# Kernel tuning notes

Hardware: AMD Instinct MI355X
Metric: run time of the kernel (lower is better)

## Reference

```python
import jax, jax.numpy as jnp
import numpy as np
from jax import lax


def squash(vec):
    # vec: [..., caps, dim]; squash along last dim (dim=2 in original layout [B, caps, dim])
    lensq = jnp.sum(vec * vec, axis=2)
    length = jnp.sqrt(lensq)
    scale = (lensq / (1.0 + lensq) / length)[:, :, None]
    return vec * scale


def setup_inputs() -> dict:
    key = jax.random.key(0)
    ks = jax.random.split(key, 6)
    stdv = 1.0 / np.sqrt(1152.0)
    return {
        "x": jax.random.normal(ks[0], (512, 1, 28, 28), dtype=jnp.float32),
        "conv1_w": jax.random.normal(ks[1], (256, 1, 9, 9), dtype=jnp.float32) * 0.05,
        "conv1_b": jax.random.normal(ks[2], (256,), dtype=jnp.float32) * 0.01,
        "conv2_w": jax.random.normal(ks[3], (256, 256, 9, 9), dtype=jnp.float32) * 0.01,
        "conv2_b": jax.random.normal(ks[4], (256,), dtype=jnp.float32) * 0.01,
        "caps_w": jax.random.uniform(ks[5], (1152, 8, 160), dtype=jnp.float32, minval=-stdv, maxval=stdv),
        "b_prior": jnp.zeros((1152, 10), dtype=jnp.float32),
    }


def reference(x, conv1_w, conv1_b, conv2_w, conv2_b, caps_w, b_prior):
    n_iterations = 3
    output_caps, output_dim = 10, 16
    dn = ("NCHW", "OIHW", "NCHW")

    # conv1 + relu: [N,1,28,28] -> [N,256,20,20]
    h = lax.conv_general_dilated(x, conv1_w, (1, 1), "VALID", dimension_numbers=dn)
    h = jax.nn.relu(h + conv1_b[None, :, None, None])

    # first capsule layer: conv k=9 s=2 -> [N,256,6,6]
    h = lax.conv_general_dilated(h, conv2_w, (2, 2), "VALID", dimension_numbers=dn)
    h = h + conv2_b[None, :, None, None]
    N, C, H, W = h.shape
    # [N, 32, 8, H, W] -> [N, 32, H, W, 8] -> [N, 32*H*W, 8]
    u = h.reshape(N, 32, 8, H, W).transpose(0, 1, 3, 4, 2).reshape(N, 32 * H * W, 8)
    u = squash(u)  # [N, 1152, 8]

    # prediction vectors: u_hat [N, 1152, 10, 16]
    u_hat = jnp.einsum("bid,ido->bio", u, caps_w).reshape(N, 1152, output_caps, output_dim)

    # dynamic routing-by-agreement
    c = jax.nn.softmax(b_prior, axis=1)  # [1152, 10]
    s = jnp.sum(c[None, :, :, None] * u_hat, axis=1)  # [N, 10, 16]
    v = squash(s)
    b_batch = jnp.broadcast_to(b_prior, (N, 1152, output_caps))
    for _ in range(n_iterations):
        b_batch = b_batch + jnp.sum(u_hat * v[:, None, :, :], axis=-1)  # agreement
        c = jax.nn.softmax(b_batch, axis=2)[..., None]  # [N, 1152, 10, 1]
        s = jnp.sum(c * u_hat, axis=1)
        v = squash(s)

    probs = jnp.sqrt(jnp.sum(v * v, axis=2))  # [N, 10]
    return (v, probs)
```

## Files before the change

kernel.cpp:

```cpp
#include <hip/hip_runtime.h>


#define N_IMG 512

typedef __attribute__((ext_vector_type(8))) short bf16x8;
typedef __attribute__((ext_vector_type(4))) float f32x4;
typedef __attribute__((ext_vector_type(4))) unsigned int u32x4;

__device__ __forceinline__ unsigned short f2bf(float v) {
  unsigned int uu = __float_as_uint(v);
  uu += 0x7FFF + ((uu >> 16) & 1);
  return (unsigned short)(uu >> 16);
}
__device__ __forceinline__ float bf2f(unsigned short h) {
  return __uint_as_float(((unsigned int)h) << 16);
}
__device__ __forceinline__ int swz16(int row) {
  return (row ^ ((row >> 3) & 7)) << 4;
}

__global__ __launch_bounds__(256) void repack_b_kernel(
    const float* __restrict__ w2, unsigned short* __restrict__ bph,
    unsigned short* __restrict__ bpl) {
  __shared__ float slab[82 * 16 * 17];
  const int n = blockIdx.x, c = blockIdx.y;
  const int tid = threadIdx.x;
  for (int e = tid; e < 81 * 256; e += 256) {
    const int row = e / 81;
    const int rs = e - row * 81;
    const int co = row >> 4, ci = row & 15;
    slab[(rs * 16 + co) * 17 + ci] =
        w2[((size_t)(n * 16 + co) * 256 + c * 16 + ci) * 81 + rs];
  }
  __syncthreads();
  const int lane = tid & 63;
  const int l15 = lane & 15;
  const int lh = lane >> 5;
  const int cio8 = ((lane >> 4) & 1) * 8;
  for (int tt = tid >> 6; tt < 41; tt += 4) {
    const int rs = 2 * tt + lh;
    unsigned int hw[4], lw[4];
#pragma unroll
    for (int jp = 0; jp < 4; ++jp) {
      unsigned short h2[2], l2[2];
#pragma unroll
      for (int e = 0; e < 2; ++e) {
        const int j = jp * 2 + e;
        float v = (rs < 81) ? slab[(rs * 16 + l15) * 17 + cio8 + j] : 0.0f;
        unsigned short hh = f2bf(v);
        h2[e] = hh;
        l2[e] = f2bf(v - bf2f(hh));
      }
      hw[jp] = (unsigned int)h2[0] | ((unsigned int)h2[1] << 16);
      lw[jp] = (unsigned int)l2[0] | ((unsigned int)l2[1] << 16);
    }
    const size_t off = (((size_t)n * 656 + c * 41 + tt) * 64 + lane) * 8;
    *(u32x4*)(bph + off) = (u32x4){hw[0], hw[1], hw[2], hw[3]};
    *(u32x4*)(bpl + off) = (u32x4){lw[0], lw[1], lw[2], lw[3]};
  }
}

__global__ __launch_bounds__(160) void repack_cw_kernel(
    const float* __restrict__ cw, float* __restrict__ cwt) {
  __shared__ float t[8][160];
  const int i = blockIdx.x;
  const int od = threadIdx.x;
#pragma unroll
  for (int k = 0; k < 8; ++k) t[k][od] = cw[((size_t)i * 8 + k) * 160 + od];
  __syncthreads();
  float4 o0 = {t[0][od], t[1][od], t[2][od], t[3][od]};
  float4 o1 = {t[4][od], t[5][od], t[6][od], t[7][od]};
  float4* dst = (float4*)(cwt + ((size_t)i * 160 + od) * 8);
  dst[0] = o0;
  dst[1] = o1;
}

__global__ __launch_bounds__(256) void c0_kernel(const float* __restrict__ bp,
                                                 float* __restrict__ c0b) {
  const int i = blockIdx.x * 256 + threadIdx.x;
  if (i >= 1152) return;
  float b[10];
  float m = -1e30f;
#pragma unroll
  for (int o = 0; o < 10; ++o) {
    b[o] = bp[i * 10 + o];
    m = fmaxf(m, b[o]);
  }
  float sum = 0.0f;
#pragma unroll
  for (int o = 0; o < 10; ++o) {
    b[o] = __expf(b[o] - m);
    sum += b[o];
  }
  const float inv = 1.0f / sum;
#pragma unroll
  for (int o = 0; o < 10; ++o) c0b[i * 10 + o] = b[o] * inv;
}

__global__ __launch_bounds__(256) void gemm_s0_kernel(
    const float* __restrict__ u, const float* __restrict__ cw,
    const float* __restrict__ c0b, float* __restrict__ s0p) {
  __shared__ float a_l[64 * 257];
  __shared__ float b_l[64 * 160];
  __shared__ float c0_l[320];
  const int mt = blockIdx.x;
  const int ks = blockIdx.y;
  const int m0 = mt * 64;
  const int tid = threadIdx.x;
  const int mb = tid >> 4;
  const int ob = (tid & 15) * 10;

  for (int i = tid; i < 320; i += 256) c0_l[i] = c0b[(ks * 32) * 10 + i];
  for (int idx = tid; idx < 16384; idx += 256) {
    const int m = idx >> 8, kk = idx & 255;
    a_l[m * 257 + kk] = u[(size_t)(m0 + m) * 9216 + ks * 256 + kk];
  }

  float acc[4][10];
#pragma unroll
  for (int r = 0; r < 4; ++r)
#pragma unroll
    for (int c = 0; c < 10; ++c) acc[r][c] = 0.0f;

#pragma unroll 1
  for (int kc = 0; kc < 4; ++kc) {
    __syncthreads();
    for (int idx = tid; idx < 10240; idx += 256) {
      const int kk = idx / 160, od = idx - kk * 160;
      const int kg = kc * 64 + kk;
      b_l[kk * 160 + od] = cw[((size_t)ks * 256 + kg) * 160 + od] *
                           c0_l[(kg >> 3) * 10 + (od >> 4)];
    }
    __syncthreads();
#pragma unroll 4
    for (int kk = 0; kk < 64; ++kk) {
      float a4[4];
#pragma unroll
      for (int r = 0; r < 4; ++r)
        a4[r] = a_l[(mb * 4 + r) * 257 + kc * 64 + kk];
      const float* bp_ = &b_l[kk * 160 + ob];
#pragma unroll
      for (int c = 0; c < 10; ++c) {
        const float bv = bp_[c];
#pragma unroll
        for (int r = 0; r < 4; ++r) acc[r][c] = fmaf(a4[r], bv, acc[r][c]);
      }
    }
  }

#pragma unroll
  for (int r = 0; r < 4; ++r) {
#pragma unroll
    for (int c = 0; c < 10; ++c) {
      s0p[((size_t)ks * N_IMG + m0 + mb * 4 + r) * 160 + ob + c] = acc[r][c];
    }
  }
}

template <int H>
__device__ __forceinline__ void conv1_half(const float* __restrict__ ib,
                                           const float* __restrict__ w1l,
                                           float* __restrict__ stg, int ch,
                                           int oy, float bv1) {
  float a[10];
#pragma unroll
  for (int ox = 0; ox < 10; ++ox) a[ox] = bv1;
#pragma unroll
  for (int r = 0; r < 9; ++r) {
    float row[20];
    const float4* rp = (const float4*)&ib[(oy + r) * 28 + H * 8];
#pragma unroll
    for (int q = 0; q < 5; ++q) {
      float4 v4 = rp[q];
      row[4 * q + 0] = v4.x; row[4 * q + 1] = v4.y;
      row[4 * q + 2] = v4.z; row[4 * q + 3] = v4.w;
    }
#pragma unroll
    for (int s = 0; s < 9; ++s) {
      const float wval = w1l[ch * 81 + r * 9 + s];
#pragma unroll
      for (int ox = 0; ox < 10; ++ox)
        a[ox] = fmaf(row[ox + s + 2 * H], wval, a[ox]);
    }
  }
  float2* dst = (float2*)&stg[oy * 20 + H * 10];
#pragma unroll
  for (int q = 0; q < 5; ++q) {
    float2 v2;
    v2.x = fmaxf(a[2 * q + 0], 0.0f);
    v2.y = fmaxf(a[2 * q + 1], 0.0f);
    dst[q] = v2;
  }
}

__global__ __launch_bounds__(512, 1) void fused_conv_kernel(
    const float* __restrict__ x, const float* __restrict__ w1,
    const float* __restrict__ b1, const unsigned short* __restrict__ bph,
    const unsigned short* __restrict__ bpl, const float* __restrict__ b2,
    float* __restrict__ u) {
  __shared__ __align__(16) char smem[115008];
  float* stg = (float*)(smem + 51776);
  float* img = (float*)(smem + 103488);
  float* w1l = (float*)(smem + 109760);
  float* b1l = (float*)(smem + 114944);
  float* mrg = (float*)smem;
  float* sq = (float*)smem;

  const int bp2 = blockIdx.x;
  const int tid = threadIdx.x;
  const int wid = tid >> 6;
  const int g = wid & 3;
  const int kpar = wid >> 2;
  const int lane = tid & 63;
  const int l15 = lane & 15;
  const int lq4 = lane >> 4;
  const int lqb = lq4 & 1;
  const int lh = lane >> 5;

  int rowb[5];
  bool okm[5];
#pragma unroll
  for (int mt = 0; mt < 5; ++mt) {
    const int m = mt * 16 + l15;
    okm[mt] = (m < 72);
    const int mm = okm[mt] ? m : 0;
    const int im = (mm >= 36) ? 1 : 0;
    const int p = mm - 36 * im;
    const int oy = p / 6, ox = p - 6 * oy;
    rowb[mt] = im * 400 + 40 * oy + 2 * ox;
  }

  for (int i = tid; i < 1568; i += 512) img[i] = x[bp2 * 1568 + i];
  if (tid < 16) {
    *(int*)(smem + (tid >> 2) * 12944 + 804 * 16 + (tid & 3) * 4) = 0;
  }

  f32x4 acc[5][4];
#pragma unroll
  for (int mt = 0; mt < 5; ++mt)
#pragma unroll
    for (int nn = 0; nn < 4; ++nn) acc[mt][nn] = (f32x4){0.f, 0.f, 0.f, 0.f};

  const char* hbase = smem + lqb * 12944;
  const char* lbase = smem + 25888 + lqb * 12944;
  const int tt0 = kpar ? 21 : 0;
  const int tt1 = kpar ? 41 : 21;
  const int nk = tt1 - tt0;

#define MFMA_STEP(CBH, CBL, J, DOPF)                                       \
  {                                                                        \
    const int rs_ = 2 * (tt0 + (J)) + lh;                                  \
    const int r_ = (rs_ * 57) >> 9;                                        \
    const int s_ = rs_ - 9 * r_;                                           \
    const int rs20_ = 20 * r_ + s_;                                        \
    const bool okrs_ = (rs_ <= 80);                                        \
    bf16x8 ah[5], al[5];                                                   \
    _Pragma("unroll") for (int mt = 0; mt < 5; ++mt) {                     \
      const int row_ = (okm[mt] && okrs_) ? (rowb[mt] + rs20_) : 800;      \
      const int ad_ = swz16(row_);                                         \
      ah[mt] = *(const bf16x8*)(hbase + ad_);                              \
      al[mt] = *(const bf16x8*)(lbase + ad_);                              \
    }                                                                      \
    _Pragma("unroll") for (int mt = 0; mt < 5; ++mt) {                     \
      _Pragma("unroll") for (int nn = 0; nn < 4; ++nn) {                   \
        acc[mt][nn] = __builtin_amdgcn_mfma_f32_16x16x32_bf16(             \
            al[mt], CBH[nn], acc[mt][nn], 0, 0, 0);                        \
        acc[mt][nn] = __builtin_amdgcn_mfma_f32_16x16x32_bf16(             \
            ah[mt], CBL[nn], acc[mt][nn], 0, 0, 0);                        \
        acc[mt][nn] = __builtin_amdgcn_mfma_f32_16x16x32_bf16(             \
            ah[mt], CBH[nn], acc[mt][nn], 0, 0, 0);                        \
      }                                                                    \
    }                                                                      \
    if ((DOPF) && (J) + 2 < nk) {                                          \
      _Pragma("unroll") for (int nn = 0; nn < 4; ++nn) {                   \
        CBH[nn] = *(const bf16x8*)(pb[nn] + (size_t)((J) + 2) * 512);      \
        CBL[nn] = *(const bf16x8*)(pl[nn] + (size_t)((J) + 2) * 512);      \
      }                                                                    \
    }                                                                      \
  }

#pragma unroll 1
  for (int c = 0; c < 16; ++c) {
    const unsigned short* pb[4];
    const unsigned short* pl[4];
#pragma unroll
    for (int nn = 0; nn < 4; ++nn) {
      const size_t base =
          ((size_t)(g * 4 + nn) * 656 + c * 41 + tt0) * 512 + lane * 8;
      pb[nn] = bph + base;
      pl[nn] = bpl + base;
    }
    bf16x8 cbh0[4], cbl0[4], cbh1[4], cbl1[4];
#pragma unroll
    for (int nn = 0; nn < 4; ++nn) {
      cbh0[nn] = *(const bf16x8*)(pb[nn]);
      cbl0[nn] = *(const bf16x8*)(pl[nn]);
      cbh1[nn] = *(const bf16x8*)(pb[nn] + 512);
      cbl1[nn] = *(const bf16x8*)(pl[nn] + 512);
    }

    __syncthreads();
    for (int i = tid; i < 1296; i += 512) w1l[i] = w1[c * 1296 + i];
    if (tid < 16) b1l[tid] = b1[c * 16 + tid];
    __syncthreads();

    for (int t = tid; t < 1280; t += 512) {
      const int half = (t >= 640) ? 1 : 0;
      const int rest = t - half * 640;
      const int ig = rest / 320;
      const int r2 = rest - ig * 320;
      const int ch = r2 & 15;
      const int oy = r2 >> 4;
      const float* ib = &img[ig * 784];
      float* sb = &stg[(ig * 16 + ch) * 404];
      const float bv1 = b1l[ch];
      if (half == 0)
        conv1_half<0>(ib, w1l, sb, ch, oy, bv1);
      else
        conv1_half<1>(ib, w1l, sb, ch, oy, bv1);
    }
    __syncthreads();

    for (int t = tid; t < 800; t += 512) {
      const int ig = t / 400;
      const int pos = t - ig * 400;
      const int ad = swz16(t);
      unsigned int hw[8], lw[8];
#pragma unroll
      for (int jp = 0; jp < 8; ++jp) {
        unsigned short h2[2], l2[2];
#pragma unroll
        for (int e = 0; e < 2; ++e) {
          const float v = stg[(ig * 16 + jp * 2 + e) * 404 + pos];
          const unsigned short hh = f2bf(v);
          h2[e] = hh;
          l2[e] = f2bf(v - bf2f(hh));
        }
        hw[jp] = (unsigned int)h2[0] | ((unsigned int)h2[1] << 16);
        lw[jp] = (unsigned int)l2[0] | ((unsigned int)l2[1] << 16);
      }
      *(u32x4*)(smem + ad) = (u32x4){hw[0], hw[1], hw[2], hw[3]};
      *(u32x4*)(smem + 12944 + ad) = (u32x4){hw[4], hw[5], hw[6], hw[7]};
      *(u32x4*)(smem + 25888 + ad) = (u32x4){lw[0], lw[1], lw[2], lw[3]};
      *(u32x4*)(smem + 38832 + ad) = (u32x4){lw[4], lw[5], lw[6], lw[7]};
    }
    __syncthreads();

    int j = 0;
#pragma unroll 1
    for (; j + 1 < nk; j += 2) {
      MFMA_STEP(cbh0, cbl0, j, 1);
      MFMA_STEP(cbh1, cbl1, j + 1, 1);
    }
    if (j < nk) MFMA_STEP(cbh0, cbl0, j, 0);
  }
#undef MFMA_STEP

  __syncthreads();
  if (kpar == 1) {
#pragma unroll
    for (int mt = 0; mt < 5; ++mt)
#pragma unroll
      for (int nn = 0; nn < 4; ++nn)
        *(f32x4*)(mrg + ((((g * 5 + mt) * 4 + nn) * 64 + lane) << 2)) =
            acc[mt][nn];
  }
  __syncthreads();
  if (kpar == 0) {
#pragma unroll
    for (int mt = 0; mt < 5; ++mt)
#pragma unroll
      for (int nn = 0; nn < 4; ++nn)
        acc[mt][nn] +=
            *(const f32x4*)(mrg + ((((g * 5 + mt) * 4 + nn) * 64 + lane) << 2));
  }
  __syncthreads();
  if (kpar == 0) {
    float b2v[4];
#pragma unroll
    for (int nn = 0; nn < 4; ++nn) b2v[nn] = b2[(g * 4 + nn) * 16 + l15];
#pragma unroll
    for (int mt = 0; mt < 5; ++mt) {
#pragma unroll
      for (int i = 0; i < 4; ++i) {
        const int m = mt * 16 + lq4 * 4 + i;
        if (m < 72) {
          const int im = (m >= 36) ? 1 : 0;
          const int p36 = m - 36 * im;
#pragma unroll
          for (int nn = 0; nn < 4; ++nn) {
            sq[(im * 256 + (g * 4 + nn) * 16 + l15) * 36 + p36] =
                acc[mt][nn][i] + b2v[nn];
          }
        }
      }
    }
  }
  __syncthreads();

  for (int i = tid; i < 2304; i += 512) {
    const int ig = i / 1152;
    const int cap = i - ig * 1152;
    const int gg = cap / 36, yx = cap - 36 * gg;
    float vals[8];
    float lensq = 0.0f;
#pragma unroll
    for (int d = 0; d < 8; ++d) {
      vals[d] = sq[(ig * 256 + gg * 8 + d) * 36 + yx];
      lensq = fmaf(vals[d], vals[d], lensq);
    }
    const float len = sqrtf(lensq);
    const float scale = lensq / (1.0f + lensq) / len;
    float4* dst = (float4*)(u + ((size_t)(bp2 * 2 + ig) * 1152 + cap) * 8);
    float4 lo4, hi4;
    lo4.x = vals[0] * scale; lo4.y = vals[1] * scale;
    lo4.z = vals[2] * scale; lo4.w = vals[3] * scale;
    hi4.x = vals[4] * scale; hi4.y = vals[5] * scale;
    hi4.z = vals[6] * scale; hi4.w = vals[7] * scale;
    dst[0] = lo4; dst[1] = hi4;
  }
}

__global__ __launch_bounds__(256) void routing_a_kernel(
    const float* __restrict__ u, const float* __restrict__ cwt,
    const float* __restrict__ b_prior, const float* __restrict__ vsum,
    float* __restrict__ s_part, int pass) {
  __shared__ float u_l[64 * 8];
  __shared__ float uhat[64 * 160];
  __shared__ float b_l[64 * 10];
  __shared__ float c_l[64 * 10];
  __shared__ float v_l[160];

  const int b = blockIdx.x;
  const int ch = blockIdx.y;
  const int cap0 = ch * 64;
  const int tid = threadIdx.x;

  {
    const float* src = u + ((size_t)b * 1152 + cap0) * 8;
    for (int i = tid; i < 512; i += 256) u_l[i] = src[i];
  }
  if (pass > 0 && tid < 160) v_l[tid] = vsum[b * 160 + tid];
  __syncthreads();

  for (int idx = tid; idx < 64 * 160; idx += 256) {
    const int i = idx / 160, od = idx - 160 * i;
    const float4* wp =
        (const float4*)(cwt + ((size_t)(cap0 + i) * 160 + od) * 8);
    const float4 wa = wp[0], wb = wp[1];
    const float4 ua = *(const float4*)&u_l[i * 8];
    const float4 ub = *(const float4*)&u_l[i * 8 + 4];
    float a = ua.x * wa.x;
    a = fmaf(ua.y, wa.y, a); a = fmaf(ua.z, wa.z, a); a = fmaf(ua.w, wa.w, a);
    a = fmaf(ub.x, wb.x, a); a = fmaf(ub.y, wb.y, a);
    a = fmaf(ub.z, wb.z, a); a = fmaf(ub.w, wb.w, a);
    uhat[idx] = a;
  }
  __syncthreads();

  for (int idx = tid; idx < 640; idx += 256) {
    const int i = idx / 10, o = idx - 10 * i;
    float bb = b_prior[(cap0 + i) * 10 + o];
    if (pass > 0) {
      float agg = 0.0f;
#pragma unroll
      for (int d = 0; d < 16; ++d)
        agg = fmaf(uhat[i * 160 + o * 16 + d], v_l[o * 16 + d], agg);
      bb += agg;
    }
    b_l[idx] = bb;
  }
  __syncthreads();

  if (tid < 64) {
    float m = -1e30f;
#pragma unroll
    for (int o = 0; o < 10; ++o) m = fmaxf(m, b_l[tid * 10 + o]);
    float e[10], sum = 0.0f;
#pragma unroll
    for (int o = 0; o < 10; ++o) {
      e[o] = __expf(b_l[tid * 10 + o] - m);
      sum += e[o];
    }
    const float inv = 1.0f / sum;
#pragma unroll
    for (int o = 0; o < 10; ++o) c_l[tid * 10 + o] = e[o] * inv;
  }
  __syncthreads();

  if (tid < 160) {
    const int o = tid / 16;
    float a = 0.0f;
    for (int i = 0; i < 64; ++i)
      a = fmaf(c_l[i * 10 + o], uhat[i * 160 + tid], a);
    s_part[((size_t)ch * N_IMG + b) * 160 + tid] = a;
  }
}

__global__ __launch_bounds__(192) void routing_b_kernel(
    const float* __restrict__ s_part, int nchunk, float* __restrict__ v_out,
    float* __restrict__ probs, float* __restrict__ vsum, int mode) {
  __shared__ float s_l[160];
  __shared__ float scale_l[10];
  __shared__ float len_l[10];
  const int b = blockIdx.x;
  const int t = threadIdx.x;
  if (t < 160) {
    float a = 0.0f;
    for (int ch = 0; ch < nchunk; ++ch)
      a += s_part[((size_t)ch * N_IMG + b) * 160 + t];
    s_l[t] = a;
  }
  __syncthreads();
  if (t < 10) {
    float lensq = 0.0f;
#pragma unroll
    for (int d = 0; d < 16; ++d) {
      const float xv = s_l[t * 16 + d];
      lensq = fmaf(xv, xv, lensq);
    }
    const float len = sqrtf(lensq);
    scale_l[t] = lensq / (1.0f + lensq) / len;
    len_l[t] = lensq / (1.0f + lensq);
  }
  __syncthreads();
  if (t < 160) {
    const float vv = s_l[t] * scale_l[t / 16];
    v_out[b * 160 + t] = vv;
    if (mode == 0) vsum[b * 160 + t] = vv;
    else if (mode == 1) vsum[b * 160 + t] += vv;
  }
  if (t < 10) probs[b * 10 + t] = len_l[t];
}

extern "C" void kernel_launch(void* const* d_in, const int* in_sizes, int n_in,
                              void* d_out, int out_size, void* d_ws,
                              size_t ws_size, hipStream_t stream) {
  const float* x  = (const float*)d_in[0];
  const float* w1 = (const float*)d_in[1];
  const float* b1 = (const float*)d_in[2];
  const float* w2 = (const float*)d_in[3];
  const float* b2 = (const float*)d_in[4];
  const float* cw = (const float*)d_in[5];
  const float* bp = (const float*)d_in[6];

  float* out = (float*)d_out;
  float* v_out = out;
  float* probs = out + N_IMG * 160;

  float* base = (float*)d_ws;
  unsigned short* bph = (unsigned short*)d_ws;
  unsigned short* bpl = bph + (size_t)16 * 656 * 512;
  float* u    = base + 5373952;
  float* sp   = u + 4718592;
  float* vsum = sp + 1474560;
  float* c0b  = vsum + 81920;
  float* cwt = base;
  float* s0p = base + 1474560;

  repack_b_kernel<<<dim3(16, 16), 256, 0, stream>>>(w2, bph, bpl);
  fused_conv_kernel<<<256, 512, 0, stream>>>(x, w1, b1, bph, bpl, b2, u);
  c0_kernel<<<5, 256, 0, stream>>>(bp, c0b);
  repack_cw_kernel<<<1152, 160, 0, stream>>>(cw, cwt);
  gemm_s0_kernel<<<dim3(8, 36), 256, 0, stream>>>(u, cw, c0b, s0p);
  routing_b_kernel<<<N_IMG, 192, 0, stream>>>(s0p, 36, v_out, probs, vsum, 0);
  for (int pass = 1; pass < 4; ++pass) {
    const int mode = (pass < 3) ? 1 : 2;
    routing_a_kernel<<<dim3(N_IMG, 18), 256, 0, stream>>>(u, cwt, bp, vsum, sp,
                                                          pass);
    routing_b_kernel<<<N_IMG, 192, 0, stream>>>(sp, 18, v_out, probs, vsum,
                                                mode);
  }
}
```

Baseline: 1.104 ms.

## Batch four images per routing block to reuse capsule weights across images

Each routing_a block now handles RG=4 images and 32 capsules, walked in two 16-capsule sub-chunks. Each loaded cwt weight vector is reused across the four images, so weight traffic per image drops. The padded uhat layout, with rows of 161, is meant to reduce LDS bank conflicts. The grid goes to 128x36 blocks with partial sums over 36 chunks, which adds more work to the reduction in routing_b and changes the workspace layout.

```diff
diff --git a/kernel.cpp b/kernel.cpp
--- a/kernel.cpp
+++ b/kernel.cpp
@@ -2,6 +2,7 @@
 
 
 #define N_IMG 512
+#define RG 4
 
 typedef __attribute__((ext_vector_type(8))) short bf16x8;
 typedef __attribute__((ext_vector_type(4))) float f32x4;
@@ -424,76 +425,106 @@
 __global__ __launch_bounds__(256) void routing_a_kernel(
     const float* __restrict__ u, const float* __restrict__ cwt,
     const float* __restrict__ b_prior, const float* __restrict__ vsum,
-    float* __restrict__ s_part, int pass) {
-  __shared__ float u_l[64 * 8];
-  __shared__ float uhat[64 * 160];
-  __shared__ float b_l[64 * 10];
-  __shared__ float c_l[64 * 10];
-  __shared__ float v_l[160];
-
-  const int b = blockIdx.x;
+    float* __restrict__ s_part) {
+  __shared__ float u_l[RG * 16 * 8];
+  __shared__ float uhat[RG][16][161];
+  __shared__ float v_l[RG * 160];
+  __shared__ float bp_l[32 * 10];
+  __shared__ float c_l[RG * 16 * 10];
+  __shared__ float s_acc[RG * 160];
+
+  const int gb = blockIdx.x;
   const int ch = blockIdx.y;
-  const int cap0 = ch * 64;
+  const int cap0 = ch * 32;
+  const int b0 = gb * RG;
   const int tid = threadIdx.x;
 
-  {
-    const float* src = u + ((size_t)b * 1152 + cap0) * 8;
-    for (int i = tid; i < 512; i += 256) u_l[i] = src[i];
-  }
-  if (pass > 0 && tid < 160) v_l[tid] = vsum[b * 160 + tid];
-  __syncthreads();
-
-  for (int idx = tid; idx < 64 * 160; idx += 256) {
-    const int i = idx / 160, od = idx - 160 * i;
-    const float4* wp =
-        (const float4*)(cwt + ((size_t)(cap0 + i) * 160 + od) * 8);
-    const float4 wa = wp[0], wb = wp[1];
-    const float4 ua = *(const float4*)&u_l[i * 8];
-    const float4 ub = *(const float4*)&u_l[i * 8 + 4];
-    float a = ua.x * wa.x;
-    a = fmaf(ua.y, wa.y, a); a = fmaf(ua.z, wa.z, a); a = fmaf(ua.w, wa.w, a);
-    a = fmaf(ub.x, wb.x, a); a = fmaf(ub.y, wb.y, a);
-    a = fmaf(ub.z, wb.z, a); a = fmaf(ub.w, wb.w, a);
-    uhat[idx] = a;
-  }
-  __syncthreads();
-
-  for (int idx = tid; idx < 640; idx += 256) {
-    const int i = idx / 10, o = idx - 10 * i;
-    float bb = b_prior[(cap0 + i) * 10 + o];
-    if (pass > 0) {
+  for (int i = tid; i < RG * 160; i += 256) {
+    const int g = i / 160, od = i - g * 160;
+    v_l[i] = vsum[(b0 + g) * 160 + od];
+    s_acc[i] = 0.0f;
+  }
+  for (int i = tid; i < 320; i += 256) bp_l[i] = b_prior[cap0 * 10 + i];
+
+#pragma unroll 1
+  for (int cc = 0; cc < 2; ++cc) {
+    const int c16 = cap0 + cc * 16;
+    __syncthreads();
+    for (int i = tid; i < RG * 128; i += 256) {
+      const int g = i >> 7, off = i & 127;
+      u_l[g * 128 + off] = u[((size_t)(b0 + g) * 1152 + c16) * 8 + off];
+    }
+    __syncthreads();
+
+    for (int e = tid; e < 2560; e += 256) {
+      const int i = e / 160, od = e - i * 160;
+      const float4* wp =
+          (const float4*)(cwt + ((size_t)(c16 + i) * 160 + od) * 8);
+      const float4 wa = wp[0], wb = wp[1];
+#pragma unroll
+      for (int g = 0; g < RG; ++g) {
+        const float* up = &u_l[(g * 16 + i) * 8];
+        float a = up[0] * wa.x;
+        a = fmaf(up[1], wa.y, a);
+        a = fmaf(up[2], wa.z, a);
+        a = fmaf(up[3], wa.w, a);
+        a = fmaf(up[4], wb.x, a);
+        a = fmaf(up[5], wb.y, a);
+        a = fmaf(up[6], wb.z, a);
+        a = fmaf(up[7], wb.w, a);
+        uhat[g][i][od] = a;
+      }
+    }
+    __syncthreads();
+
+    for (int e = tid; e < RG * 160; e += 256) {
+      const int g = e / 160;
+      const int r = e - g * 160;
+      const int i = r / 10, o = r - i * 10;
       float agg = 0.0f;
 #pragma unroll
       for (int d = 0; d < 16; ++d)
-        agg = fmaf(uhat[i * 160 + o * 16 + d], v_l[o * 16 + d], agg);
-      bb += agg;
-    }
-    b_l[idx] = bb;
-  }
-  __syncthreads();
-
-  if (tid < 64) {
-    float m = -1e30f;
-#pragma unroll
-    for (int o = 0; o < 10; ++o) m = fmaxf(m, b_l[tid * 10 + o]);
-    float e[10], sum = 0.0f;
-#pragma unroll
-    for (int o = 0; o < 10; ++o) {
-      e[o] = __expf(b_l[tid * 10 + o] - m);
-      sum += e[o];
-    }
-    const float inv = 1.0f / sum;
-#pragma unroll
-    for (int o = 0; o < 10; ++o) c_l[tid * 10 + o] = e[o] * inv;
-  }
-  __syncthreads();
-
-  if (tid < 160) {
-    const int o = tid / 16;
-    float a = 0.0f;
-    for (int i = 0; i < 64; ++i)
-      a = fmaf(c_l[i * 10 + o], uhat[i * 160 + tid], a);
-    s_part[((size_t)ch * N_IMG + b) * 160 + tid] = a;
+        agg = fmaf(uhat[g][i][o * 16 + d], v_l[g * 160 + o * 16 + d], agg);
+      c_l[e] = bp_l[(cc * 16 + i) * 10 + o] + agg;
+    }
+    __syncthreads();
+
+    if (tid < RG * 16) {
+      const int g = tid >> 4, i = tid & 15;
+      float bb[10];
+      float m = -1e30f;
+#pragma unroll
+      for (int o = 0; o < 10; ++o) {
+        bb[o] = c_l[(g * 16 + i) * 10 + o];
+        m = fmaxf(m, bb[o]);
+      }
+      float sum = 0.0f;
+#pragma unroll
+      for (int o = 0; o < 10; ++o) {
+        bb[o] = __expf(bb[o] - m);
+        sum += bb[o];
+      }
+      const float inv = 1.0f / sum;
+#pragma unroll
+      for (int o = 0; o < 10; ++o) c_l[(g * 16 + i) * 10 + o] = bb[o] * inv;
+    }
+    __syncthreads();
+
+    for (int e = tid; e < RG * 160; e += 256) {
+      const int g = e / 160, od = e - g * 160;
+      const int o = od >> 4;
+      float a = 0.0f;
+#pragma unroll
+      for (int i = 0; i < 16; ++i)
+        a = fmaf(c_l[(g * 16 + i) * 10 + o], uhat[g][i][od], a);
+      s_acc[e] += a;
+    }
+  }
+  __syncthreads();
+
+  for (int e = tid; e < RG * 160; e += 256) {
+    const int g = e / 160, od = e - g * 160;
+    s_part[((size_t)ch * N_IMG + b0 + g) * 160 + od] = s_acc[e];
   }
 }
 
@@ -552,23 +583,22 @@
   unsigned short* bph = (unsigned short*)d_ws;
   unsigned short* bpl = bph + (size_t)16 * 656 * 512;
   float* u    = base + 5373952;
-  float* sp   = u + 4718592;
-  float* vsum = sp + 1474560;
+  float* vsum = u + 4718592;
   float* c0b  = vsum + 81920;
   float* cwt = base;
-  float* s0p = base + 1474560;
+  float* sp  = base + 1474560;
 
   repack_b_kernel<<<dim3(16, 16), 256, 0, stream>>>(w2, bph, bpl);
   fused_conv_kernel<<<256, 512, 0, stream>>>(x, w1, b1, bph, bpl, b2, u);
   c0_kernel<<<5, 256, 0, stream>>>(bp, c0b);
   repack_cw_kernel<<<1152, 160, 0, stream>>>(cw, cwt);
-  gemm_s0_kernel<<<dim3(8, 36), 256, 0, stream>>>(u, cw, c0b, s0p);
-  routing_b_kernel<<<N_IMG, 192, 0, stream>>>(s0p, 36, v_out, probs, vsum, 0);
+  gemm_s0_kernel<<<dim3(8, 36), 256, 0, stream>>>(u, cw, c0b, sp);
+  routing_b_kernel<<<N_IMG, 192, 0, stream>>>(sp, 36, v_out, probs, vsum, 0);
   for (int pass = 1; pass < 4; ++pass) {
     const int mode = (pass < 3) ? 1 : 2;
-    routing_a_kernel<<<dim3(N_IMG, 18), 256, 0, stream>>>(u, cwt, bp, vsum, sp,
-                                                          pass);
-    routing_b_kernel<<<N_IMG, 192, 0, stream>>>(sp, 18, v_out, probs, vsum,
+    routing_a_kernel<<<dim3(N_IMG / RG, 36), 256, 0, stream>>>(u, cwt, bp,
+                                                               vsum, sp);
+    routing_b_kernel<<<N_IMG, 192, 0, stream>>>(sp, 36, v_out, probs, vsum,
                                                 mode);
   }
 }
```

New measurement: 1.017 ms (median of 3 runs). 1.09x faster.
